# Kernel tuning notes

Measured on AMD Instinct MI355X. Metric: run time of the kernel, lower is better.

The kernel has to match this reference:

```python
import jax, jax.numpy as jnp
import numpy as np

NUM_CLASSES = 2
THRESHOLD = 0.35
NEGPOS_RATIO = 7
VARIANCES = (0.1, 0.2)
B, P, O = 64, 16800, 64  # batch, num_priors, num_objs per image


def point_form(pr):
    # cxcywh -> xyxy
    return jnp.concatenate([pr[:, :2] - pr[:, 2:] / 2, pr[:, :2] + pr[:, 2:] / 2], axis=1)


def jaccard(a, b):
    # a: [A,4] xyxy, b: [Bx,4] xyxy -> IoU [A,Bx]
    lt = jnp.maximum(a[:, None, :2], b[None, :, :2])
    rb = jnp.minimum(a[:, None, 2:], b[None, :, 2:])
    wh = jnp.clip(rb - lt, 0.0)
    inter = wh[..., 0] * wh[..., 1]
    area_a = ((a[:, 2] - a[:, 0]) * (a[:, 3] - a[:, 1]))[:, None]
    area_b = ((b[:, 2] - b[:, 0]) * (b[:, 3] - b[:, 1]))[None, :]
    return inter / (area_a + area_b - inter)


def encode(matched, priors):
    # matched xyxy [P,4], priors cxcywh [P,4]
    g_cxcy = (matched[:, :2] + matched[:, 2:]) / 2 - priors[:, :2]
    g_cxcy = g_cxcy / (VARIANCES[0] * priors[:, 2:])
    g_wh = (matched[:, 2:] - matched[:, :2]) / priors[:, 2:]
    g_wh = jnp.log(g_wh) / VARIANCES[1]
    return jnp.concatenate([g_cxcy, g_wh], axis=1)


def encode_landm(matched, priors):
    # matched [P,10] -> [P,5,2]
    m = matched.reshape(-1, 5, 2)
    g = (m - priors[:, None, :2]) / (VARIANCES[0] * priors[:, None, 2:])
    return g.reshape(-1, 10)


def match_one(truths, labels, landms, priors):
    # truths [O,4], labels [O], landms [O,10]
    overlaps = jaccard(truths, point_form(priors))  # [O,P]
    best_prior_overlap = overlaps.max(axis=1)       # per-gt best IoU
    best_prior_idx = overlaps.argmax(axis=1)
    valid_gt = best_prior_overlap >= 0.2
    best_truth_overlap = overlaps.max(axis=0)       # per-prior best IoU
    best_truth_idx = overlaps.argmax(axis=0)
    # index_fill(2) only for valid gts (best_prior_idx_filter)
    bto = best_truth_overlap.at[best_prior_idx].set(
        jnp.where(valid_gt, 2.0, best_truth_overlap[best_prior_idx]))
    # ensure every gt keeps its best prior
    bti = best_truth_idx.at[best_prior_idx].set(jnp.arange(truths.shape[0]))
    matches = truths[bti]                  # [P,4]
    conf = labels[bti]                     # [P]
    conf = jnp.where(bto < THRESHOLD, 0.0, conf)
    loc = encode(matches, priors)
    landm = encode_landm(landms[bti], priors)
    return loc, conf, landm


def smooth_l1_sum(x, mask):
    ax = jnp.abs(x)
    v = jnp.where(ax < 1.0, 0.5 * ax * ax, ax - 0.5)
    return (v * mask).sum()


def setup_inputs() -> dict:
    key = jax.random.key(0)
    k1, k2, k3, k4, k5, k6, k7, k8 = jax.random.split(key, 8)
    loc_data = jax.random.normal(k1, (B, P, 4), jnp.float32)
    conf_data = jax.random.normal(k2, (B, P, NUM_CLASSES), jnp.float32)
    landm_data = jax.random.normal(k3, (B, P, 10), jnp.float32)
    # priors: cx,cy in (0,1), w,h in (0.02,0.22)
    cxy = jax.random.uniform(k4, (P, 2), jnp.float32)
    wh = jax.random.uniform(k5, (P, 2), jnp.float32) * 0.2 + 0.02
    priors = jnp.concatenate([cxy, wh], axis=1)
    # targets: valid corner boxes + landmarks + label in {1,-1}
    xy1 = jax.random.uniform(k6, (B, O, 2), jnp.float32) * 0.6
    bwh = jax.random.uniform(k7, (B, O, 2), jnp.float32) * 0.3 + 0.05
    boxes = jnp.concatenate([xy1, xy1 + bwh], axis=-1)
    lms = jax.random.uniform(k8, (B, O, 10), jnp.float32)
    lab = jnp.where(jax.random.uniform(jax.random.fold_in(key, 9), (B, O, 1)) < 0.3, -1.0, 1.0)
    targets = jnp.concatenate([boxes, lms, lab], axis=-1)
    return {"loc_data": loc_data, "conf_data": conf_data, "landm_data": landm_data,
            "priors": priors, "targets": targets}


def reference(loc_data, conf_data, landm_data, priors, targets):
    num = loc_data.shape[0]
    num_priors = priors.shape[0]
    truths = targets[:, :, :4]
    landms = targets[:, :, 4:14]
    labels = targets[:, :, -1]
    loc_t, conf_t, landm_t = jax.vmap(match_one, in_axes=(0, 0, 0, None))(
        truths, labels, landms, priors)  # [B,P,4], [B,P], [B,P,10]

    # landmark loss over conf_t > 0
    pos1 = conf_t > 0
    num_pos_landm = pos1.astype(jnp.int32).sum(axis=1, keepdims=True)
    N1 = jnp.maximum(num_pos_landm.sum().astype(jnp.float32), 1.0)
    loss_landm = smooth_l1_sum(landm_data - landm_t, pos1[..., None].astype(landm_data.dtype))

    # localization loss over conf_t != 0 ; conf_t[pos] = 1
    pos = conf_t != 0
    conf_t01 = jnp.where(pos, 1, 0)  # int {0,1}
    loss_l = smooth_l1_sum(loc_data - loc_t, pos[..., None].astype(loc_data.dtype))

    # hard negative mining on per-prior CE loss (global-max log_sum_exp, as in source)
    batch_conf = conf_data.reshape(-1, NUM_CLASSES)
    x_max = batch_conf.max()
    lse = jnp.log(jnp.exp(batch_conf - x_max).sum(axis=1, keepdims=True)) + x_max
    gathered = jnp.take_along_axis(batch_conf, conf_t01.reshape(-1, 1), axis=1)
    loss_c = (lse - gathered).reshape(num, -1)  # [B,P]; positives NOT zeroed (as in source)
    loss_idx = jnp.argsort(-loss_c, axis=1)
    idx_rank = jnp.argsort(loss_idx, axis=1)
    num_pos = pos.astype(jnp.int32).sum(axis=1, keepdims=True)  # [B,1]
    num_neg = jnp.minimum(NEGPOS_RATIO * num_pos, num_priors - 1)
    neg = idx_rank < num_neg  # [B,P]
    neg_pos = pos | neg

    # cross-entropy (sum) over selected pos+neg priors
    logp = jax.nn.log_softmax(conf_data, axis=-1)  # [B,P,C]
    ce = -jnp.take_along_axis(logp, conf_t01[..., None], axis=-1)[..., 0]
    loss_c_final = (ce * neg_pos.astype(ce.dtype)).sum()

    N = jnp.maximum(num_pos.sum().astype(jnp.float32), 1.0)
    return (loss_l / N, loss_c_final / N, loss_landm / N1)
```

## Files before the change

### kernel.cpp

```cpp
#include <hip/hip_runtime.h>
#include <math.h>

#define BN 64
#define PN 16800
#define ON 64
#define THRESH 0.35f
#define NEGPOS 7
#define GX 66
#define NBLK (BN * GX)
#define NBP 1024
#define NCELL 256
#define NCB 66
#define EPSW 0.0009765625f
#define IOUF 0.3499f
#define NBINS 4096
#define MAXM 4096
#define TAILT 104

struct GAcc {
  unsigned ticket;
  float sl, slm, sc;
  int np, np1;
  unsigned pad0, pad1;
};

__device__ __forceinline__ unsigned f2key(float f) {
  unsigned u = __float_as_uint(f);
  return (u & 0x80000000u) ? ~u : (u | 0x80000000u);
}
__device__ __forceinline__ float key2f(unsigned k) {
  unsigned u = (k & 0x80000000u) ? (k & 0x7FFFFFFFu) : ~k;
  return __uint_as_float(u);
}
__device__ __forceinline__ float sl1(float d) {
  float a = fabsf(d);
  return (a < 1.f) ? 0.5f * a * a : a - 0.5f;
}

__global__ void k_count(const float* __restrict__ priors,
                        unsigned char* __restrict__ pcell,
                        unsigned* __restrict__ gcnt,
                        unsigned* __restrict__ gmax) {
  __shared__ unsigned lcnt[NCELL];
  int tid = threadIdx.x;
  lcnt[tid] = 0;
  __syncthreads();
  int p = blockIdx.x * 256 + tid;
  float mw = 0.f, mh = 0.f;
  if (p < PN) {
    float4 pr = reinterpret_cast<const float4*>(priors)[p];
    int cx = (int)(pr.x * 16.f); cx = cx < 0 ? 0 : (cx > 15 ? 15 : cx);
    int cy = (int)(pr.y * 16.f); cy = cy < 0 ? 0 : (cy > 15 ? 15 : cy);
    int cell = cy * 16 + cx;
    pcell[p] = (unsigned char)cell;
    atomicAdd(&lcnt[cell], 1u);
    mw = pr.z * 0.5f;
    mh = pr.w * 0.5f;
  }
#pragma unroll
  for (int off = 32; off; off >>= 1) {
    mw = fmaxf(mw, __shfl_xor(mw, off));
    mh = fmaxf(mh, __shfl_xor(mh, off));
  }
  if ((tid & 63) == 0) {
    atomicMax(&gmax[0], __float_as_uint(mw));
    atomicMax(&gmax[1], __float_as_uint(mh));
  }
  __syncthreads();
  unsigned c = lcnt[tid];
  if (c) atomicAdd(&gcnt[tid], c);
}

__global__ void k_scatter(const float* __restrict__ priors,
                          const float* __restrict__ targets,
                          const unsigned char* __restrict__ pcell,
                          const unsigned* __restrict__ gcnt,
                          unsigned* __restrict__ gcur,
                          const unsigned* __restrict__ gmax,
                          float4* __restrict__ sbox,
                          int* __restrict__ sorig,
                          int* __restrict__ cellOff,
                          unsigned long long* __restrict__ tmask) {
  int bid = blockIdx.x;
  int tid = threadIdx.x;
  if (bid < NCB) {
    __shared__ unsigned tmp[NCELL];
    __shared__ unsigned excl[NCELL];
    __shared__ unsigned lcnt[NCELL];
    __shared__ unsigned lbase[NCELL];
    unsigned c = gcnt[tid];
    tmp[tid] = c;
    lcnt[tid] = 0;
    __syncthreads();
    for (int off = 1; off < NCELL; off <<= 1) {
      unsigned v = (tid >= off) ? tmp[tid - off] : 0u;
      __syncthreads();
      tmp[tid] += v;
      __syncthreads();
    }
    excl[tid] = tmp[tid] - c;
    if (bid == 0) {
      cellOff[tid] = (int)(tmp[tid] - c);
      if (tid == 0) cellOff[NCELL] = PN;
    }
    __syncthreads();
    int p = bid * 256 + tid;
    bool valid = p < PN;
    int cell = 0; unsigned lrank = 0;
    if (valid) {
      cell = pcell[p];
      lrank = atomicAdd(&lcnt[cell], 1u);
    }
    __syncthreads();
    if (lcnt[tid]) lbase[tid] = atomicAdd(&gcur[tid], lcnt[tid]);
    __syncthreads();
    if (valid) {
      int slot = (int)(excl[cell] + lbase[cell] + lrank);
      float4 pr = reinterpret_cast<const float4*>(priors)[p];
      float px1 = pr.x - pr.z * 0.5f, py1 = pr.y - pr.w * 0.5f;
      float px2 = pr.x + pr.z * 0.5f, py2 = pr.y + pr.w * 0.5f;
      sbox[slot] = make_float4(px1, py1, px2, py2);
      sorig[slot] = p;
    }
  } else {
    int b = bid - NCB;
    __shared__ float4 tb[ON];
    if (tid < ON) {
      const float* tg = &targets[((long)b * ON + tid) * 15];
      tb[tid] = make_float4(tg[0], tg[1], tg[2], tg[3]);
    }
    __syncthreads();
    float MW = __uint_as_float(gmax[0]), MH = __uint_as_float(gmax[1]);
    int cx = tid & 15, cy = tid >> 4;
    float cxl = (float)cx * 0.0625f, cxh = (float)(cx + 1) * 0.0625f;
    float cyl = (float)cy * 0.0625f, cyh = (float)(cy + 1) * 0.0625f;
    float pmaxa = 4.f * MW * MH;
    unsigned long long m = 0ull;
    for (int t = 0; t < ON; t++) {
      float4 a = tb[t];
      float wt = a.z - a.x, ht = a.w - a.y;
      float at = wt * ht;
      float need = IOUF * at;
      float wmin = need / fminf(ht, 2.f * MH);
      float hmin = need / fminf(wt, 2.f * MW);
      float wx0 = a.x + wmin - MW - EPSW, wx1 = a.z - wmin + MW + EPSW;
      float wy0 = a.y + hmin - MH - EPSW, wy1 = a.w - hmin + MH + EPSW;
      bool ok = (pmaxa >= need) &&
                (cxh > wx0) && (cxl < wx1) &&
                (cyh > wy0) && (cyl < wy1);
      if (ok) m |= (1ull << t);
    }
    tmask[b * NCELL + tid] = m;
  }
}

__global__ void k_bp(const float* __restrict__ targets,
                     const float4* __restrict__ sbox,
                     const int* __restrict__ sorig,
                     const int* __restrict__ cellOff,
                     const unsigned* __restrict__ gmax,
                     unsigned long long* __restrict__ bpp) {
  int bid = blockIdx.x;
  int tid = threadIdx.x;
  int lane = tid & 63, wv = tid >> 6;
  int b = bid >> 4;
  int t = ((bid & 15) << 2) + wv;
  const float* tg = &targets[((long)b * ON + t) * 15];
  float ax1 = tg[0], ay1 = tg[1], ax2 = tg[2], ay2 = tg[3];
  float aa = (ax2 - ax1) * (ay2 - ay1);
  float MW = __uint_as_float(gmax[0]), MH = __uint_as_float(gmax[1]);
  int xlo = (int)floorf((ax1 - MW - EPSW) * 16.f); xlo = xlo < 0 ? 0 : (xlo > 15 ? 15 : xlo);
  int xhi = (int)floorf((ax2 + MW + EPSW) * 16.f); xhi = xhi < 0 ? 0 : (xhi > 15 ? 15 : xhi);
  int ylo = (int)floorf((ay1 - MH - EPSW) * 16.f); ylo = ylo < 0 ? 0 : (ylo > 15 ? 15 : ylo);
  int yhi = (int)floorf((ay2 + MH + EPSW) * 16.f); yhi = yhi < 0 ? 0 : (yhi > 15 ? 15 : yhi);
  float bi = 0.f, bu = 1.f; int bp = 0;
  for (int cy = ylo; cy <= yhi; cy++) {
    int s0 = cellOff[cy * 16 + xlo];
    int s1 = cellOff[cy * 16 + xhi + 1];
    for (int s = s0 + lane; s < s1; s += 64) {
      float4 pr = sbox[s];
      int op = sorig[s];
      float ab2 = (pr.z - pr.x) * (pr.w - pr.y);
      float lx = fmaxf(ax1, pr.x), ly = fmaxf(ay1, pr.y);
      float rx = fminf(ax2, pr.z), ry = fminf(ay2, pr.w);
      float w = fmaxf(rx - lx, 0.f), h = fmaxf(ry - ly, 0.f);
      float inter = w * h;
      float uni = aa + ab2 - inter;
      float A = inter * bu, C = bi * uni;
      if (A > C || (A == C && op < bp)) { bi = inter; bu = uni; bp = op; }
    }
  }
#pragma unroll
  for (int off = 1; off < 64; off <<= 1) {
    float oi = __shfl_xor(bi, off), ou = __shfl_xor(bu, off);
    int op = __shfl_xor(bp, off);
    float A = oi * bu, C = bi * ou;
    if (A > C || (A == C && op < bp)) { bi = oi; bu = ou; bp = op; }
  }
  if (lane == 0) {
    float q = bi / bu;
    bpp[(long)b * ON + t] = ((unsigned long long)f2key(q) << 32) | (unsigned)(~bp);
  }
}

__global__ void k_encode(const float* __restrict__ loc_data,
                         const float* __restrict__ conf_data,
                         const float* __restrict__ landm_data,
                         const float* __restrict__ priors,
                         const float* __restrict__ targets,
                         const unsigned char* __restrict__ pcell,
                         const unsigned long long* __restrict__ tmask,
                         const unsigned long long* __restrict__ bpp,
                         float* __restrict__ lossc, unsigned char* __restrict__ posf,
                         float* __restrict__ part_l, float* __restrict__ part_lm,
                         int* __restrict__ np_part, int* __restrict__ np1_part) {
  int b = blockIdx.y;
  int p = blockIdx.x * 256 + threadIdx.x;
  int bid = b * GX + blockIdx.x;
  __shared__ float4 tgs4[ON * 15 / 4];
  __shared__ float4 tb[ON];
  __shared__ float ta[ON];
  __shared__ unsigned long long smask[NCELL];
  __shared__ int ovr[256];
  float* tgs = (float*)tgs4;
  if (threadIdx.x < ON * 15 / 4)
    tgs4[threadIdx.x] = reinterpret_cast<const float4*>(targets + (long)b * ON * 15)[threadIdx.x];
  smask[threadIdx.x] = tmask[b * NCELL + threadIdx.x];
  if (threadIdx.x < ON) {
    const float* tg = &targets[((long)b * ON + threadIdx.x) * 15];
    float4 bx = make_float4(tg[0], tg[1], tg[2], tg[3]);
    tb[threadIdx.x] = bx;
    ta[threadIdx.x] = (bx.z - bx.x) * (bx.w - bx.y);
  }
  ovr[threadIdx.x] = -1;
  __syncthreads();
  if (threadIdx.x < ON) {
    int t = threadIdx.x;
    unsigned long long best = bpp[(long)b * ON + t];
    float q = key2f((unsigned)(best >> 32));
    int qp = (int)(~(unsigned)best);
    int s0 = blockIdx.x * 256;
    if (qp >= s0 && qp < s0 + 256) {
      int valid = (q >= 0.2f) ? 1 : 0;
      atomicMax(&ovr[qp - s0], (t << 1) | valid);
    }
  }
  __syncthreads();

  float sum_l = 0.f, sum_lm = 0.f;
  int cp = 0, cp1 = 0;
  if (p < PN) {
    float4 pr = reinterpret_cast<const float4*>(priors)[p];
    float px1 = pr.x - pr.z * 0.5f, py1 = pr.y - pr.w * 0.5f;
    float px2 = pr.x + pr.z * 0.5f, py2 = pr.y + pr.w * 0.5f;
    float ab2 = (px2 - px1) * (py2 - py1);
    unsigned long long m = smask[pcell[p]];
    float bi = 0.f, bu = 1.f; int t = 0;
    while (m) {
      int t0 = __builtin_ctzll(m); m &= m - 1;
      float4 a0 = tb[t0];
      float lx = fmaxf(a0.x, px1), ly = fmaxf(a0.y, py1);
      float rx = fminf(a0.z, px2), ry = fminf(a0.w, py2);
      float w2 = fmaxf(rx - lx, 0.f), h2 = fmaxf(ry - ly, 0.f);
      float inter = w2 * h2;
      float uni = ta[t0] + ab2 - inter;
      if (inter * bu > bi * uni) { bi = inter; bu = uni; t = t0; }
    }
    bool pos = (bi / bu) >= THRESH;
    int o = ovr[threadIdx.x];
    if (o >= 0) { t = o >> 1; if (o & 1) pos = true; }
    const float* tg = &tgs[t * 15];
    float label = tg[14];
    bool pos1 = pos && (label > 0.f);
    if (pos) {
      float rz = 1.0f / pr.z, rw = 1.0f / pr.w;
      float m0 = tg[0], m1 = tg[1], m2 = tg[2], m3 = tg[3];
      float g0 = ((m0 + m2) * 0.5f - pr.x) * rz * 10.f;
      float g1 = ((m1 + m3) * 0.5f - pr.y) * rw * 10.f;
      float g2 = __logf((m2 - m0) * rz) * 5.f;
      float g3 = __logf((m3 - m1) * rw) * 5.f;
      const float* ld = &loc_data[((long)b * PN + p) * 4];
      sum_l = sl1(ld[0] - g0) + sl1(ld[1] - g1) + sl1(ld[2] - g2) + sl1(ld[3] - g3);
      cp = 1;
      if (pos1) {
        const float* lm = &landm_data[((long)b * PN + p) * 10];
#pragma unroll
        for (int i = 0; i < 5; i++) {
          float gx = (tg[4 + 2 * i] - pr.x) * rz * 10.f;
          float gy = (tg[5 + 2 * i] - pr.y) * rw * 10.f;
          sum_lm += sl1(lm[2 * i] - gx) + sl1(lm[2 * i + 1] - gy);
        }
        cp1 = 1;
      }
    }
    float2 c2 = reinterpret_cast<const float2*>(conf_data)[(long)b * PN + p];
    float mx = fmaxf(c2.x, c2.y);
    float lse = mx + __logf(__expf(c2.x - mx) + __expf(c2.y - mx));
    lossc[b * PN + p] = lse - (pos ? c2.y : c2.x);
    posf[b * PN + p] = pos ? 1 : 0;
  }
  for (int off = 32; off; off >>= 1) {
    sum_l += __shfl_down(sum_l, off);
    sum_lm += __shfl_down(sum_lm, off);
    cp += __shfl_down(cp, off);
    cp1 += __shfl_down(cp1, off);
  }
  __shared__ float sl4[4], slm4[4];
  __shared__ int sp4[4], sp14[4];
  int w = threadIdx.x >> 6;
  if ((threadIdx.x & 63) == 0) { sl4[w] = sum_l; slm4[w] = sum_lm; sp4[w] = cp; sp14[w] = cp1; }
  __syncthreads();
  if (threadIdx.x == 0) {
    part_l[bid] = sl4[0] + sl4[1] + sl4[2] + sl4[3];
    part_lm[bid] = slm4[0] + slm4[1] + slm4[2] + slm4[3];
    np_part[bid] = sp4[0] + sp4[1] + sp4[2] + sp4[3];
    np1_part[bid] = sp14[0] + sp14[1] + sp14[2] + sp14[3];
  }
}

__global__ void __launch_bounds__(1024) k_select(const float* __restrict__ lossc,
                                                 const unsigned char* __restrict__ posf,
                                                 const int* __restrict__ np_part,
                                                 const int* __restrict__ np1_part,
                                                 const float* __restrict__ part_l,
                                                 const float* __restrict__ part_lm,
                                                 GAcc* __restrict__ gacc,
                                                 float* __restrict__ out) {
  int b = blockIdx.x;
  int tid = threadIdx.x;
  int lane = tid & 63;
  int wv = tid >> 6;
  __shared__ unsigned hist[NBINS];
  __shared__ unsigned wtot[16];
  __shared__ float resv[MAXM];
  __shared__ int residx[MAXM];
  __shared__ int s_np, s_B, s_kp;
  __shared__ unsigned s_mc;
  const float* row = &lossc[(long)b * PN];
  const unsigned char* prow = &posf[(long)b * PN];

  if (tid == 0) s_np = 0;
  for (int i = tid; i < NBINS; i += 1024) hist[i] = 0;
  __syncthreads();
  if (tid < GX) atomicAdd(&s_np, np_part[b * GX + tid]);

  const float4* rf4 = reinterpret_cast<const float4*>(row);
  const uint4* pw4 = reinterpret_cast<const uint4*>(prow);
  bool hasTail = tid < TAILT;
  float vm[16];
  float vt[4];
  {
    float4 L0 = rf4[tid * 4], L1 = rf4[tid * 4 + 1], L2 = rf4[tid * 4 + 2], L3 = rf4[tid * 4 + 3];
    vm[0] = L0.x; vm[1] = L0.y; vm[2] = L0.z; vm[3] = L0.w;
    vm[4] = L1.x; vm[5] = L1.y; vm[6] = L1.z; vm[7] = L1.w;
    vm[8] = L2.x; vm[9] = L2.y; vm[10] = L2.z; vm[11] = L2.w;
    vm[12] = L3.x; vm[13] = L3.y; vm[14] = L3.z; vm[15] = L3.w;
  }
  unsigned pmask = 0;
  {
    uint4 W = pw4[tid];
    unsigned w0 = W.x, w1 = W.y, w2 = W.z, w3 = W.w;
#pragma unroll
    for (int j = 0; j < 4; j++) {
      pmask |= ((w0 >> (8 * j)) & 1u) << j;
      pmask |= ((w1 >> (8 * j)) & 1u) << (4 + j);
      pmask |= ((w2 >> (8 * j)) & 1u) << (8 + j);
      pmask |= ((w3 >> (8 * j)) & 1u) << (12 + j);
    }
  }
  unsigned tmask = 0;
  if (hasTail) {
    float4 Lt = rf4[4096 + tid];
    vt[0] = Lt.x; vt[1] = Lt.y; vt[2] = Lt.z; vt[3] = Lt.w;
    unsigned Wt = reinterpret_cast<const unsigned*>(prow)[4096 + tid];
#pragma unroll
    for (int j = 0; j < 4; j++) tmask |= ((Wt >> (8 * j)) & 1u) << j;
  } else {
    vt[0] = vt[1] = vt[2] = vt[3] = -1.f;
  }
  int bm[16], bt4[4];
#pragma unroll
  for (int j = 0; j < 16; j++) {
    int q = (int)(vm[j] * 256.0f);
    bm[j] = q < 0 ? 0 : (q > NBINS - 1 ? NBINS - 1 : q);
  }
#pragma unroll
  for (int j = 0; j < 4; j++) {
    int q = (int)(vt[j] * 256.0f);
    bt4[j] = q < 0 ? 0 : (q > NBINS - 1 ? NBINS - 1 : q);
  }
  __syncthreads();
  int np = s_np;
  int k = NEGPOS * np;
  if (k > PN - 1) k = PN - 1;
  bool haveNeg = (k > 0);

  int B = NBINS, kp = 0, m = 0;
  bool allB = false, fallback = false;
  if (haveNeg) {
#pragma unroll
    for (int j = 0; j < 16; j++) atomicAdd(&hist[bm[j]], 1u);
    if (hasTail) {
#pragma unroll
      for (int j = 0; j < 4; j++) atomicAdd(&hist[bt4[j]], 1u);
    }
    __syncthreads();
    int t4 = tid * 4;
    unsigned h0 = hist[t4], h1 = hist[t4 + 1], h2 = hist[t4 + 2], h3 = hist[t4 + 3];
    unsigned th = h0 + h1 + h2 + h3;
    unsigned v = th;
#pragma unroll
    for (int off = 1; off < 64; off <<= 1) {
      unsigned tv = (unsigned)__shfl_down((int)v, off);
      if (lane + off < 64) v += tv;
    }
    if (lane == 0) wtot[wv] = v;
    __syncthreads();
    unsigned add = 0;
    for (int w2 = wv + 1; w2 < 16; w2++) add += wtot[w2];
    unsigned S_t = v + add;
    unsigned S_next = S_t - th;
    if (S_t >= (unsigned)k && S_next < (unsigned)k) {
      unsigned run = S_next; int Bl; unsigned kpl;
      if (run + h3 >= (unsigned)k) { Bl = t4 + 3; kpl = k - run; }
      else { run += h3;
        if (run + h2 >= (unsigned)k) { Bl = t4 + 2; kpl = k - run; }
        else { run += h2;
          if (run + h1 >= (unsigned)k) { Bl = t4 + 1; kpl = k - run; }
          else { run += h1; Bl = t4; kpl = k - run; } } }
      s_B = Bl; s_kp = (int)kpl;
    }
    __syncthreads();
    B = s_B; kp = s_kp; m = (int)hist[B];
    allB = (kp == m);
    fallback = (!allB && m > MAXM);
  }

  float acc = 0.f;
  if (haveNeg && !allB && !fallback) {
    if (tid == 0) s_mc = 0;
    __syncthreads();
#pragma unroll
    for (int j = 0; j < 16; j++) {
      if (bm[j] == B) {
        unsigned slot = atomicAdd(&s_mc, 1u);
        resv[slot] = vm[j];
        residx[slot] = (tid * 16 + j) | (((pmask >> j) & 1u) ? 0x40000000 : 0);
      }
    }
    if (hasTail) {
#pragma unroll
      for (int j = 0; j < 4; j++) {
        if (bt4[j] == B) {
          unsigned slot = atomicAdd(&s_mc, 1u);
          resv[slot] = vt[j];
          residx[slot] = (16384 + tid * 4 + j) | (((tmask >> j) & 1u) ? 0x40000000 : 0);
        }
      }
    }
    __syncthreads();
    for (int i = tid; i < m; i += 1024) {
      float vi = resv[i];
      int pk = residx[i];
      int ii = pk & 0x3FFFFFFF;
      bool posi = (pk & 0x40000000) != 0;
      int rank = 0;
      for (int j = 0; j < m; j++) {
        float vj = resv[j];
        int ij = residx[j] & 0x3FFFFFFF;
        rank += (vj > vi || (vj == vi && ij < ii)) ? 1 : 0;
      }
      if (rank < kp && !posi) acc += vi;
    }
  }

  unsigned T = 0, R = 0, C = 0;
  if (fallback) {
    __shared__ unsigned s_lo, s_hi, fcnt[16];
    if (tid == 0) { s_lo = 0u; s_hi = 0xFFFFFFFFu; }
    __syncthreads();
    for (int it = 0; it < 32; it++) {
      unsigned lo = s_lo, hi = s_hi;
      unsigned mid = lo + ((hi - lo) >> 1) + ((hi - lo) & 1u);
      unsigned c = 0;
#pragma unroll
      for (int j = 0; j < 16; j++) c += (f2key(vm[j]) >= mid) ? 1u : 0u;
      if (hasTail) {
#pragma unroll
        for (int j = 0; j < 4; j++) c += (f2key(vt[j]) >= mid) ? 1u : 0u;
      }
#pragma unroll
      for (int o = 32; o; o >>= 1) c += (unsigned)__shfl_down((int)c, o);
      if (lane == 0) fcnt[wv] = c;
      __syncthreads();
      if (tid == 0) {
        unsigned tot = 0;
        for (int i = 0; i < 16; i++) tot += fcnt[i];
        if (tot >= (unsigned)k) s_lo = mid; else s_hi = mid - 1;
      }
      __syncthreads();
      if (s_lo >= s_hi) break;
    }
    T = s_lo;
    unsigned cg = 0, ce = 0;
#pragma unroll
    for (int j = 0; j < 16; j++) {
      unsigned key = f2key(vm[j]);
      cg += (key > T) ? 1u : 0u;
      ce += (key == T) ? 1u : 0u;
    }
    if (hasTail) {
#pragma unroll
      for (int j = 0; j < 4; j++) {
        unsigned key = f2key(vt[j]);
        cg += (key > T) ? 1u : 0u;
        ce += (key == T) ? 1u : 0u;
      }
    }
#pragma unroll
    for (int o = 32; o; o >>= 1) {
      cg += (unsigned)__shfl_down((int)cg, o);
      ce += (unsigned)__shfl_down((int)ce, o);
    }
    if (lane == 0) { fcnt[wv] = cg; wtot[wv] = ce; }
    __syncthreads();
    if (tid == 0) {
      unsigned tg2 = 0, te = 0;
      for (int i = 0; i < 16; i++) { tg2 += fcnt[i]; te += wtot[i]; }
      fcnt[0] = tg2; wtot[0] = te;
    }
    __syncthreads();
    C = wtot[0];
    R = (unsigned)k - fcnt[0];
    if (C != R && tid < 64) {
      unsigned running = 0;
      for (int base2 = 0; base2 < PN; base2 += 64) {
        int p = base2 + tid;
        bool tie = false, pos = false;
        float v2 = 0.f;
        if (p < PN) { v2 = row[p]; tie = (f2key(v2) == T); pos = prow[p] != 0; }
        unsigned long long mm = __ballot(tie);
        if (tie) {
          unsigned rank = running + (unsigned)__popcll(mm & ((1ull << tid) - 1));
          if (rank < R && !pos) acc += v2;
        }
        running += (unsigned)__popcll(mm);
      }
    }
  }

  unsigned ptc = 0;
#pragma unroll
  for (int j = 0; j < 16; j++) {
    float v2 = vm[j];
    bool pos = (pmask >> j) & 1u;
    if (pos) acc += v2;
    else if (haveNeg) {
      if (!fallback) {
        if (bm[j] > B || (bm[j] == B && allB)) acc += v2;
      } else {
        if (f2key(v2) > T) acc += v2;
      }
    }
    if (fallback && pos && f2key(v2) == T) ptc++;
  }
  if (hasTail) {
#pragma unroll
    for (int j = 0; j < 4; j++) {
      float v2 = vt[j];
      bool pos = (tmask >> j) & 1u;
      if (pos) acc += v2;
      else if (haveNeg) {
        if (!fallback) {
          if (bt4[j] > B || (bt4[j] == B && allB)) acc += v2;
        } else {
          if (f2key(v2) > T) acc += v2;
        }
      }
      if (fallback && pos && f2key(v2) == T) ptc++;
    }
  }
  for (int o = 32; o; o >>= 1) {
    acc += __shfl_down(acc, o);
    ptc += __shfl_down(ptc, o);
  }
  __shared__ float wsum[16];
  __shared__ unsigned wpt[16];
  if (lane == 0) { wsum[wv] = acc; wpt[wv] = ptc; }
  __syncthreads();

  __shared__ float s_rsl, s_rslm;
  __shared__ int s_rnp1;
  if (tid == 0) { s_rsl = 0.f; s_rslm = 0.f; s_rnp1 = 0; }
  __syncthreads();
  if (tid < GX) {
    atomicAdd(&s_rsl, part_l[b * GX + tid]);
    atomicAdd(&s_rslm, part_lm[b * GX + tid]);
    atomicAdd(&s_rnp1, np1_part[b * GX + tid]);
  }
  __syncthreads();

  if (tid == 0) {
    float tot = 0.f; unsigned pt = 0;
    for (int i = 0; i < 16; i++) { tot += wsum[i]; pt += wpt[i]; }
    if (fallback && C == R) tot += (float)(C - pt) * key2f(T);
    atomicAdd(&gacc->sc, tot);
    atomicAdd(&gacc->sl, s_rsl);
    atomicAdd(&gacc->slm, s_rslm);
    atomicAdd(&gacc->np, np);
    atomicAdd(&gacc->np1, s_rnp1);
  }
  __threadfence();
  __shared__ int lastF;
  if (tid == 0) lastF = (atomicAdd(&gacc->ticket, 1u) == (unsigned)(BN - 1)) ? 1 : 0;
  __syncthreads();
  if (lastF && tid == 0) {
    __threadfence();
    float sl = atomicAdd(&gacc->sl, 0.f);
    float slm = atomicAdd(&gacc->slm, 0.f);
    float sc = atomicAdd(&gacc->sc, 0.f);
    int tnp = atomicAdd(&gacc->np, 0);
    int tnp1 = atomicAdd(&gacc->np1, 0);
    float N = fmaxf((float)tnp, 1.f);
    float N1 = fmaxf((float)tnp1, 1.f);
    out[0] = sl / N;
    out[1] = sc / N;
    out[2] = slm / N1;
  }
}

extern "C" void kernel_launch(void* const* d_in, const int* in_sizes, int n_in,
                              void* d_out, int out_size, void* d_ws, size_t ws_size,
                              hipStream_t stream) {
  const float* loc_data = (const float*)d_in[0];
  const float* conf_data = (const float*)d_in[1];
  const float* landm_data = (const float*)d_in[2];
  const float* priors = (const float*)d_in[3];
  const float* targets = (const float*)d_in[4];
  float* out = (float*)d_out;

  char* ws = (char*)d_ws;
  size_t off = 0;
  float* lossc = (float*)(ws + off); off += (size_t)BN * PN * 4;
  unsigned char* posf = (unsigned char*)(ws + off); off += (size_t)BN * PN;
  off = (off + 15) & ~(size_t)15;
  unsigned long long* bpp = (unsigned long long*)(ws + off); off += (size_t)BN * ON * 8;
  float* part_l = (float*)(ws + off); off += NBLK * 4;
  float* part_lm = (float*)(ws + off); off += NBLK * 4;
  int* np_part = (int*)(ws + off); off += NBLK * 4;
  int* np1_part = (int*)(ws + off); off += NBLK * 4;
  float4* sbox = (float4*)(ws + off); off += (size_t)PN * 16;
  int* sorig = (int*)(ws + off); off += (size_t)PN * 4;
  unsigned char* pcell = (unsigned char*)(ws + off); off += (size_t)PN;
  off = (off + 15) & ~(size_t)15;
  int* cellOff = (int*)(ws + off); off += 260 * 4;
  unsigned long long* tmask = (unsigned long long*)(ws + off); off += (size_t)BN * NCELL * 8;
  off = (off + 15) & ~(size_t)15;
  unsigned* zreg = (unsigned*)(ws + off);
  unsigned* gcnt = zreg;
  unsigned* gcur = zreg + 256;
  unsigned* gmax = zreg + 512;
  GAcc* gacc = (GAcc*)(zreg + 516);
  size_t zbytes = (256 + 256 + 4) * 4 + sizeof(GAcc);
  off += zbytes;

  hipMemsetAsync(zreg, 0, zbytes, stream);
  k_count<<<NCB, 256, 0, stream>>>(priors, pcell, gcnt, gmax);
  k_scatter<<<NCB + BN, 256, 0, stream>>>(priors, targets, pcell, gcnt, gcur, gmax,
                                          sbox, sorig, cellOff, tmask);
  k_bp<<<NBP, 256, 0, stream>>>(targets, sbox, sorig, cellOff, gmax, bpp);
  dim3 gbp(GX, BN);
  k_encode<<<gbp, 256, 0, stream>>>(loc_data, conf_data, landm_data, priors, targets,
                                    pcell, tmask, bpp, lossc, posf,
                                    part_l, part_lm, np_part, np1_part);
  k_select<<<BN, 1024, 0, stream>>>(lossc, posf, np_part, np1_part, part_l, part_lm,
                                    gacc, out);
}
```

Before: 206.7 us.

## Replace histogram top-k selection with radix bisection and scan-based tie ranking

The per-row hard-negative selection drops the 4096-bin shared histogram, the O(m^2) rank computation and the serial tie-walk fallback. It now always runs a 32-step bisection over float keys to find the threshold, and ranks ties with a wave-level prefix scan. The global atomic ticket accumulator is replaced by per-row partial outputs and a small final reduction kernel. This cuts shared-memory use and removes quadratic and serial paths, in exchange for a fixed bisection cost on every row and one extra kernel launch.

New measurement: 212.1 us. +2.6%, slower.

```diff
diff --git a/kernel.cpp b/kernel.cpp
--- a/kernel.cpp
+++ b/kernel.cpp
@@ -13,16 +13,7 @@
 #define NCB 66
 #define EPSW 0.0009765625f
 #define IOUF 0.3499f
-#define NBINS 4096
-#define MAXM 4096
 #define TAILT 104
-
-struct GAcc {
-  unsigned ticket;
-  float sl, slm, sc;
-  int np, np1;
-  unsigned pad0, pad1;
-};
 
 __device__ __forceinline__ unsigned f2key(float f) {
   unsigned u = __float_as_uint(f);
@@ -324,25 +315,31 @@
                                                  const int* __restrict__ np1_part,
                                                  const float* __restrict__ part_l,
                                                  const float* __restrict__ part_lm,
-                                                 GAcc* __restrict__ gacc,
-                                                 float* __restrict__ out) {
+                                                 float* __restrict__ rout) {
   int b = blockIdx.x;
   int tid = threadIdx.x;
   int lane = tid & 63;
   int wv = tid >> 6;
-  __shared__ unsigned hist[NBINS];
-  __shared__ unsigned wtot[16];
-  __shared__ float resv[MAXM];
-  __shared__ int residx[MAXM];
-  __shared__ int s_np, s_B, s_kp;
-  __shared__ unsigned s_mc;
+  __shared__ int s_np, s_rnp1;
+  __shared__ float s_rsl, s_rslm;
+  __shared__ unsigned s_lo, s_hi, s_cg, s_totp;
+  __shared__ unsigned fcnt[16];
+  __shared__ unsigned wsc[16];
+  __shared__ float wsum[16];
   const float* row = &lossc[(long)b * PN];
   const unsigned char* prow = &posf[(long)b * PN];
 
-  if (tid == 0) s_np = 0;
-  for (int i = tid; i < NBINS; i += 1024) hist[i] = 0;
-  __syncthreads();
-  if (tid < GX) atomicAdd(&s_np, np_part[b * GX + tid]);
+  if (tid == 0) {
+    s_np = 0; s_rnp1 = 0; s_rsl = 0.f; s_rslm = 0.f;
+    s_lo = 0u; s_hi = 0xFFFFFFFFu;
+  }
+  __syncthreads();
+  if (tid < GX) {
+    atomicAdd(&s_np, np_part[b * GX + tid]);
+    atomicAdd(&s_rsl, part_l[b * GX + tid]);
+    atomicAdd(&s_rslm, part_lm[b * GX + tid]);
+    atomicAdd(&s_rnp1, np1_part[b * GX + tid]);
+  }
 
   const float4* rf4 = reinterpret_cast<const float4*>(row);
   const uint4* pw4 = reinterpret_cast<const uint4*>(prow);
@@ -378,116 +375,28 @@
   } else {
     vt[0] = vt[1] = vt[2] = vt[3] = -1.f;
   }
-  int bm[16], bt4[4];
-#pragma unroll
-  for (int j = 0; j < 16; j++) {
-    int q = (int)(vm[j] * 256.0f);
-    bm[j] = q < 0 ? 0 : (q > NBINS - 1 ? NBINS - 1 : q);
-  }
-#pragma unroll
-  for (int j = 0; j < 4; j++) {
-    int q = (int)(vt[j] * 256.0f);
-    bt4[j] = q < 0 ? 0 : (q > NBINS - 1 ? NBINS - 1 : q);
-  }
+  unsigned km[16], kt4[4];
+#pragma unroll
+  for (int j = 0; j < 16; j++) km[j] = f2key(vm[j]);
+#pragma unroll
+  for (int j = 0; j < 4; j++) kt4[j] = f2key(vt[j]);
   __syncthreads();
   int np = s_np;
   int k = NEGPOS * np;
   if (k > PN - 1) k = PN - 1;
   bool haveNeg = (k > 0);
 
-  int B = NBINS, kp = 0, m = 0;
-  bool allB = false, fallback = false;
+  unsigned T = 0, Rsel = 0;
   if (haveNeg) {
-#pragma unroll
-    for (int j = 0; j < 16; j++) atomicAdd(&hist[bm[j]], 1u);
-    if (hasTail) {
-#pragma unroll
-      for (int j = 0; j < 4; j++) atomicAdd(&hist[bt4[j]], 1u);
-    }
-    __syncthreads();
-    int t4 = tid * 4;
-    unsigned h0 = hist[t4], h1 = hist[t4 + 1], h2 = hist[t4 + 2], h3 = hist[t4 + 3];
-    unsigned th = h0 + h1 + h2 + h3;
-    unsigned v = th;
-#pragma unroll
-    for (int off = 1; off < 64; off <<= 1) {
-      unsigned tv = (unsigned)__shfl_down((int)v, off);
-      if (lane + off < 64) v += tv;
-    }
-    if (lane == 0) wtot[wv] = v;
-    __syncthreads();
-    unsigned add = 0;
-    for (int w2 = wv + 1; w2 < 16; w2++) add += wtot[w2];
-    unsigned S_t = v + add;
-    unsigned S_next = S_t - th;
-    if (S_t >= (unsigned)k && S_next < (unsigned)k) {
-      unsigned run = S_next; int Bl; unsigned kpl;
-      if (run + h3 >= (unsigned)k) { Bl = t4 + 3; kpl = k - run; }
-      else { run += h3;
-        if (run + h2 >= (unsigned)k) { Bl = t4 + 2; kpl = k - run; }
-        else { run += h2;
-          if (run + h1 >= (unsigned)k) { Bl = t4 + 1; kpl = k - run; }
-          else { run += h1; Bl = t4; kpl = k - run; } } }
-      s_B = Bl; s_kp = (int)kpl;
-    }
-    __syncthreads();
-    B = s_B; kp = s_kp; m = (int)hist[B];
-    allB = (kp == m);
-    fallback = (!allB && m > MAXM);
-  }
-
-  float acc = 0.f;
-  if (haveNeg && !allB && !fallback) {
-    if (tid == 0) s_mc = 0;
-    __syncthreads();
-#pragma unroll
-    for (int j = 0; j < 16; j++) {
-      if (bm[j] == B) {
-        unsigned slot = atomicAdd(&s_mc, 1u);
-        resv[slot] = vm[j];
-        residx[slot] = (tid * 16 + j) | (((pmask >> j) & 1u) ? 0x40000000 : 0);
-      }
-    }
-    if (hasTail) {
-#pragma unroll
-      for (int j = 0; j < 4; j++) {
-        if (bt4[j] == B) {
-          unsigned slot = atomicAdd(&s_mc, 1u);
-          resv[slot] = vt[j];
-          residx[slot] = (16384 + tid * 4 + j) | (((tmask >> j) & 1u) ? 0x40000000 : 0);
-        }
-      }
-    }
-    __syncthreads();
-    for (int i = tid; i < m; i += 1024) {
-      float vi = resv[i];
-      int pk = residx[i];
-      int ii = pk & 0x3FFFFFFF;
-      bool posi = (pk & 0x40000000) != 0;
-      int rank = 0;
-      for (int j = 0; j < m; j++) {
-        float vj = resv[j];
-        int ij = residx[j] & 0x3FFFFFFF;
-        rank += (vj > vi || (vj == vi && ij < ii)) ? 1 : 0;
-      }
-      if (rank < kp && !posi) acc += vi;
-    }
-  }
-
-  unsigned T = 0, R = 0, C = 0;
-  if (fallback) {
-    __shared__ unsigned s_lo, s_hi, fcnt[16];
-    if (tid == 0) { s_lo = 0u; s_hi = 0xFFFFFFFFu; }
-    __syncthreads();
     for (int it = 0; it < 32; it++) {
       unsigned lo = s_lo, hi = s_hi;
       unsigned mid = lo + ((hi - lo) >> 1) + ((hi - lo) & 1u);
       unsigned c = 0;
 #pragma unroll
-      for (int j = 0; j < 16; j++) c += (f2key(vm[j]) >= mid) ? 1u : 0u;
+      for (int j = 0; j < 16; j++) c += (km[j] >= mid) ? 1u : 0u;
       if (hasTail) {
 #pragma unroll
-        for (int j = 0; j < 4; j++) c += (f2key(vt[j]) >= mid) ? 1u : 0u;
+        for (int j = 0; j < 4; j++) c += (kt4[j] >= mid) ? 1u : 0u;
       }
 #pragma unroll
       for (int o = 32; o; o >>= 1) c += (unsigned)__shfl_down((int)c, o);
@@ -502,127 +411,118 @@
       if (s_lo >= s_hi) break;
     }
     T = s_lo;
-    unsigned cg = 0, ce = 0;
-#pragma unroll
-    for (int j = 0; j < 16; j++) {
-      unsigned key = f2key(vm[j]);
-      cg += (key > T) ? 1u : 0u;
-      ce += (key == T) ? 1u : 0u;
-    }
+    unsigned c = 0;
+#pragma unroll
+    for (int j = 0; j < 16; j++) c += (km[j] > T) ? 1u : 0u;
     if (hasTail) {
 #pragma unroll
-      for (int j = 0; j < 4; j++) {
-        unsigned key = f2key(vt[j]);
-        cg += (key > T) ? 1u : 0u;
-        ce += (key == T) ? 1u : 0u;
-      }
-    }
-#pragma unroll
-    for (int o = 32; o; o >>= 1) {
-      cg += (unsigned)__shfl_down((int)cg, o);
-      ce += (unsigned)__shfl_down((int)ce, o);
-    }
-    if (lane == 0) { fcnt[wv] = cg; wtot[wv] = ce; }
+      for (int j = 0; j < 4; j++) c += (kt4[j] > T) ? 1u : 0u;
+    }
+#pragma unroll
+    for (int o = 32; o; o >>= 1) c += (unsigned)__shfl_down((int)c, o);
+    if (lane == 0) fcnt[wv] = c;
     __syncthreads();
     if (tid == 0) {
-      unsigned tg2 = 0, te = 0;
-      for (int i = 0; i < 16; i++) { tg2 += fcnt[i]; te += wtot[i]; }
-      fcnt[0] = tg2; wtot[0] = te;
-    }
-    __syncthreads();
-    C = wtot[0];
-    R = (unsigned)k - fcnt[0];
-    if (C != R && tid < 64) {
-      unsigned running = 0;
-      for (int base2 = 0; base2 < PN; base2 += 64) {
-        int p = base2 + tid;
-        bool tie = false, pos = false;
-        float v2 = 0.f;
-        if (p < PN) { v2 = row[p]; tie = (f2key(v2) == T); pos = prow[p] != 0; }
-        unsigned long long mm = __ballot(tie);
-        if (tie) {
-          unsigned rank = running + (unsigned)__popcll(mm & ((1ull << tid) - 1));
-          if (rank < R && !pos) acc += v2;
-        }
-        running += (unsigned)__popcll(mm);
-      }
-    }
-  }
-
-  unsigned ptc = 0;
+      unsigned tot = 0;
+      for (int i = 0; i < 16; i++) tot += fcnt[i];
+      s_cg = tot;
+    }
+    __syncthreads();
+    Rsel = (unsigned)k - s_cg;
+  }
+
+  unsigned mc = 0, tc = 0;
+  if (haveNeg) {
+#pragma unroll
+    for (int j = 0; j < 16; j++) mc += (km[j] == T) ? 1u : 0u;
+    if (hasTail) {
+#pragma unroll
+      for (int j = 0; j < 4; j++) tc += (kt4[j] == T) ? 1u : 0u;
+    }
+  }
+  unsigned packed = mc | (tc << 16);
+  unsigned inc = packed;
+#pragma unroll
+  for (int o = 1; o < 64; o <<= 1) {
+    unsigned u = (unsigned)__shfl_up((int)inc, o);
+    if (lane >= o) inc += u;
+  }
+  if (lane == 63) wsc[wv] = inc;
+  __syncthreads();
+  if (tid == 0) {
+    unsigned run = 0;
+    for (int i = 0; i < 16; i++) { unsigned t2 = wsc[i]; wsc[i] = run; run += t2; }
+    s_totp = run;
+  }
+  __syncthreads();
+  unsigned excl = wsc[wv] + inc - packed;
+  unsigned mb = excl & 0xFFFFu;
+  unsigned tb2 = (s_totp & 0xFFFFu) + (excl >> 16);
+
+  float acc = 0.f;
+  unsigned cm = 0;
 #pragma unroll
   for (int j = 0; j < 16; j++) {
     float v2 = vm[j];
     bool pos = (pmask >> j) & 1u;
     if (pos) acc += v2;
-    else if (haveNeg) {
-      if (!fallback) {
-        if (bm[j] > B || (bm[j] == B && allB)) acc += v2;
-      } else {
-        if (f2key(v2) > T) acc += v2;
+    if (haveNeg) {
+      if (km[j] > T) { if (!pos) acc += v2; }
+      else if (km[j] == T) {
+        unsigned r2 = mb + cm; cm++;
+        if (!pos && r2 < Rsel) acc += v2;
       }
     }
-    if (fallback && pos && f2key(v2) == T) ptc++;
   }
   if (hasTail) {
+    unsigned ct = 0;
 #pragma unroll
     for (int j = 0; j < 4; j++) {
       float v2 = vt[j];
       bool pos = (tmask >> j) & 1u;
       if (pos) acc += v2;
-      else if (haveNeg) {
-        if (!fallback) {
-          if (bt4[j] > B || (bt4[j] == B && allB)) acc += v2;
-        } else {
-          if (f2key(v2) > T) acc += v2;
+      if (haveNeg) {
+        if (kt4[j] > T) { if (!pos) acc += v2; }
+        else if (kt4[j] == T) {
+          unsigned r2 = tb2 + ct; ct++;
+          if (!pos && r2 < Rsel) acc += v2;
         }
       }
-      if (fallback && pos && f2key(v2) == T) ptc++;
-    }
-  }
+    }
+  }
+#pragma unroll
+  for (int o = 32; o; o >>= 1) acc += __shfl_down(acc, o);
+  if (lane == 0) wsum[wv] = acc;
+  __syncthreads();
+  if (tid == 0) {
+    float tot = 0.f;
+    for (int i = 0; i < 16; i++) tot += wsum[i];
+    rout[b * 8 + 0] = tot;
+    rout[b * 8 + 1] = s_rsl;
+    rout[b * 8 + 2] = s_rslm;
+    ((int*)rout)[b * 8 + 3] = np;
+    ((int*)rout)[b * 8 + 4] = s_rnp1;
+  }
+}
+
+__global__ void k_final(const float* __restrict__ rout, float* __restrict__ out) {
+  int tid = threadIdx.x;
+  float sc = rout[tid * 8 + 0];
+  float sl = rout[tid * 8 + 1];
+  float slm = rout[tid * 8 + 2];
+  int np = ((const int*)rout)[tid * 8 + 3];
+  int np1 = ((const int*)rout)[tid * 8 + 4];
+#pragma unroll
   for (int o = 32; o; o >>= 1) {
-    acc += __shfl_down(acc, o);
-    ptc += __shfl_down(ptc, o);
-  }
-  __shared__ float wsum[16];
-  __shared__ unsigned wpt[16];
-  if (lane == 0) { wsum[wv] = acc; wpt[wv] = ptc; }
-  __syncthreads();
-
-  __shared__ float s_rsl, s_rslm;
-  __shared__ int s_rnp1;
-  if (tid == 0) { s_rsl = 0.f; s_rslm = 0.f; s_rnp1 = 0; }
-  __syncthreads();
-  if (tid < GX) {
-    atomicAdd(&s_rsl, part_l[b * GX + tid]);
-    atomicAdd(&s_rslm, part_lm[b * GX + tid]);
-    atomicAdd(&s_rnp1, np1_part[b * GX + tid]);
-  }
-  __syncthreads();
-
+    sc += __shfl_down(sc, o);
+    sl += __shfl_down(sl, o);
+    slm += __shfl_down(slm, o);
+    np += __shfl_down(np, o);
+    np1 += __shfl_down(np1, o);
+  }
   if (tid == 0) {
-    float tot = 0.f; unsigned pt = 0;
-    for (int i = 0; i < 16; i++) { tot += wsum[i]; pt += wpt[i]; }
-    if (fallback && C == R) tot += (float)(C - pt) * key2f(T);
-    atomicAdd(&gacc->sc, tot);
-    atomicAdd(&gacc->sl, s_rsl);
-    atomicAdd(&gacc->slm, s_rslm);
-    atomicAdd(&gacc->np, np);
-    atomicAdd(&gacc->np1, s_rnp1);
-  }
-  __threadfence();
-  __shared__ int lastF;
-  if (tid == 0) lastF = (atomicAdd(&gacc->ticket, 1u) == (unsigned)(BN - 1)) ? 1 : 0;
-  __syncthreads();
-  if (lastF && tid == 0) {
-    __threadfence();
-    float sl = atomicAdd(&gacc->sl, 0.f);
-    float slm = atomicAdd(&gacc->slm, 0.f);
-    float sc = atomicAdd(&gacc->sc, 0.f);
-    int tnp = atomicAdd(&gacc->np, 0);
-    int tnp1 = atomicAdd(&gacc->np1, 0);
-    float N = fmaxf((float)tnp, 1.f);
-    float N1 = fmaxf((float)tnp1, 1.f);
+    float N = fmaxf((float)np, 1.f);
+    float N1 = fmaxf((float)np1, 1.f);
     out[0] = sl / N;
     out[1] = sc / N;
     out[2] = slm / N1;
@@ -656,12 +556,13 @@
   int* cellOff = (int*)(ws + off); off += 260 * 4;
   unsigned long long* tmask = (unsigned long long*)(ws + off); off += (size_t)BN * NCELL * 8;
   off = (off + 15) & ~(size_t)15;
+  float* rout = (float*)(ws + off); off += (size_t)BN * 8 * 4;
+  off = (off + 15) & ~(size_t)15;
   unsigned* zreg = (unsigned*)(ws + off);
   unsigned* gcnt = zreg;
   unsigned* gcur = zreg + 256;
   unsigned* gmax = zreg + 512;
-  GAcc* gacc = (GAcc*)(zreg + 516);
-  size_t zbytes = (256 + 256 + 4) * 4 + sizeof(GAcc);
+  size_t zbytes = (256 + 256 + 4) * 4;
   off += zbytes;
 
   hipMemsetAsync(zreg, 0, zbytes, stream);
@@ -674,5 +575,6 @@
                                     pcell, tmask, bpp, lossc, posf,
                                     part_l, part_lm, np_part, np1_part);
   k_select<<<BN, 1024, 0, stream>>>(lossc, posf, np_part, np1_part, part_l, part_lm,
-                                    gacc, out);
-}
+                                    rout);
+  k_final<<<1, 64, 0, stream>>>(rout, out);
+}
```
